# Performance work log

Hardware: AMD Instinct MI355X
Metric: run time of the kernel (lower is better)

## Reference

```python
import jax, jax.numpy as jnp
import numpy as np

B, V, C = 8192, 512, 16  # batch, num_variables, constraints per variable
N1 = V + 1  # augmented with bias column


def setup_inputs() -> dict:
    key = jax.random.key(0)
    k1, k2, k3 = jax.random.split(key, 3)
    preds = jax.random.normal(k1, (B, V), dtype=jnp.float32)
    # Acyclic structure: variable v's constraints only reference earlier
    # variables (columns < v) plus the bias column (column V).
    cols = jnp.arange(N1)[None, :]              # [1, N1]
    vids = jnp.arange(V)[:, None]               # [V, 1]
    mask = ((cols < vids) | (cols == V)).astype(jnp.float32)[:, None, :]  # [V,1,N1]
    scale = 0.1
    pos_mats = jax.random.normal(k2, (V, C, N1), dtype=jnp.float32) * scale * mask
    neg_mats = jax.random.normal(k3, (V, C, N1), dtype=jnp.float32) * scale * mask
    return {"preds": preds, "pos_mats": pos_mats, "neg_mats": neg_mats}


def reference(preds, pos_mats, neg_mats):
    # Augment preds with a ones column (bias), as in the original __call__.
    b = preds.shape[0]
    p0 = jnp.concatenate([preds, jnp.ones((b, 1), preds.dtype)], axis=1)  # [B, N1]
    var_ids = jnp.arange(pos_mats.shape[0])

    def step(p, xs):
        pm, nm, v = xs  # pm, nm: [C, N1]
        # apply_matrix: (preds * matrix).sum(-1) with max / min reduction over C
        lower = jnp.einsum('bn,cn->bc', p, pm).max(axis=1)  # [B]
        upper = jnp.einsum('bn,cn->bc', p, nm).min(axis=1)  # [B]
        # get_final_x_correction: clamp prediction into [lower, upper]
        corrected = jnp.minimum(jnp.maximum(p[:, v], lower), upper)
        p = p.at[:, v].set(corrected)
        return p, None

    pf, _ = jax.lax.scan(step, p0, (pos_mats, neg_mats, var_ids))
    return pf[:, : preds.shape[1]]
```

## Files before the change

### kernel.cpp

```cpp
#include <hip/hip_runtime.h>

#define BATCH 8192
#define V 512
#define N1 513
#define KCH 16
#define NCHUNKS 32
#define RB 32
#define NT 1024
#define PKS 520
#define SJ 516

typedef __bf16 bf16_t;
typedef bf16_t bf16x8 __attribute__((ext_vector_type(8)));
typedef float f32x4 __attribute__((ext_vector_type(4)));
typedef float f32x2 __attribute__((ext_vector_type(2)));

#define EPP 4194304ull
#define DV_OFF (EPP * 2ull)
#define BV_OFF (DV_OFF + 1048576ull)

__device__ __forceinline__ f32x4 mfma16(bf16x8 a, bf16x8 b, f32x4 c) {
    return __builtin_amdgcn_mfma_f32_16x16x32_bf16(a, b, c, 0, 0, 0);
}

__global__ __launch_bounds__(256)
void repack_all(const float* __restrict__ pos, const float* __restrict__ neg,
                bf16_t* __restrict__ Mhi, float* __restrict__ Dv,
                float* __restrict__ Bv)
{
    const int bx = blockIdx.x;
    if (bx < 496) {
        const int cc  = (bx >> 4) + 1;
        const int kb  = bx & 15;
        const int nkb = (cc + 1) >> 1;
        if (kb >= nkb) return;
        const int klen = 16 * cc;
        const size_t base = 16384ull * (size_t)((cc * cc) / 4) + (size_t)kb * 16384ull;
        for (int e = threadIdx.x; e < 16384; e += 256) {
            const int t = e >> 9, s = (e >> 3) & 63, jj = e & 7;
            const int c = s & 15, q = s >> 4;
            const int v = cc * 16 + (t >> 1);
            const int k = kb * 32 + 8 * q + jj;
            const float* src = (t & 1) ? neg : pos;
            float x = (k < klen) ? src[(size_t)(v * 16 + c) * N1 + k] : 0.0f;
            if (t & 1) x = -x;
            Mhi[base + e] = (bf16_t)x;
        }
    } else {
        const int e = (bx - 496) * 256 + threadIdx.x;
        if (e < 262144) {
            const int cc = e >> 13, vl = (e >> 9) & 15, j = e & 511;
            const int v = cc * 16 + (j >> 5), c = j & 15;
            const float* src = (j & 16) ? neg : pos;
            const float x = src[(size_t)(v * 16 + c) * N1 + cc * 16 + vl];
            Dv[e] = (j & 16) ? -x : x;
        } else {
            const int e2 = e - 262144;
            const int cc = e2 >> 9, j = e2 & 511;
            const int v = cc * 16 + (j >> 5), c = j & 15;
            const float* src = (j & 16) ? neg : pos;
            const float x = src[(size_t)(v * 16 + c) * N1 + V];
            Bv[e2] = (j & 16) ? -x : x;
        }
    }
}

__global__ __launch_bounds__(NT)
void shield_fused(const float* __restrict__ preds,
                  const bf16_t* __restrict__ Mhi,
                  const float* __restrict__ Dv, const float* __restrict__ Bv,
                  float* __restrict__ out)
{
    __shared__ bf16_t Phi[RB * PKS];
    __shared__ float  S[RB * SJ];

    const int tid  = threadIdx.x;
    const int b0   = blockIdx.x * RB;
    const int lane = tid & 63;
    const int w    = tid >> 6;
    const int cq   = lane & 15;
    const int q    = lane >> 4;
    const int rp0  = w * 2;

    {
        const int r = tid >> 5, seg = tid & 31;
        const float* prow = preds + (size_t)(b0 + r) * V + seg * 16;
        #pragma unroll
        for (int k = 0; k < 16; k += 4) {
            const float4 p4 = *(const float4*)(prow + k);
            const int n = seg * 16 + k;
            Phi[r * PKS + n + 0] = (bf16_t)p4.x;
            Phi[r * PKS + n + 1] = (bf16_t)p4.y;
            Phi[r * PKS + n + 2] = (bf16_t)p4.z;
            Phi[r * PKS + n + 3] = (bf16_t)p4.w;
        }
    }

    int tJ[2];
    #pragma unroll
    for (int tt = 0; tt < 2; ++tt) tJ[tt] = ((2 * w + tt) << 4) + cq;
    const int aoff0 = cq * PKS + 8 * q;
    const int aoff1 = (16 + cq) * PKS + 8 * q;

    f32x4 acc[2][2];
    #pragma unroll
    for (int tt = 0; tt < 2; ++tt) {
        const float b = Bv[tJ[tt]];
        acc[0][tt] = f32x4{b, b, b, b};
        acc[1][tt] = f32x4{b, b, b, b};
    }

    #pragma unroll 1
    for (int cc = 0; cc < NCHUNKS; ++cc) {
        const int v0 = cc * 16;
        const int  ccn  = cc + 1;
        const bool hasN = ccn < NCHUNKS;
        const int  nkbN = hasN ? ((ccn + 1) >> 1) : 0;
        const bf16_t* phN = Mhi + 16384ull * (size_t)((ccn * ccn) / 4)
                          + (size_t)lane * 8 + (size_t)(2 * w) * 512;

        #pragma unroll
        for (int tt = 0; tt < 2; ++tt)
            #pragma unroll
            for (int reg = 0; reg < 4; ++reg) {
                S[(4 * q + reg) * SJ + tJ[tt]]      = acc[0][tt][reg];
                S[(16 + 4 * q + reg) * SJ + tJ[tt]] = acc[1][tt][reg];
            }
        __syncthreads();

        f32x2 s2[8];
        {
            const float4 a0 = *(const float4*)(&S[rp0 * SJ + 8 * lane]);
            const float4 a1 = *(const float4*)(&S[rp0 * SJ + 8 * lane + 4]);
            const float4 c0 = *(const float4*)(&S[(rp0 + 1) * SJ + 8 * lane]);
            const float4 c1 = *(const float4*)(&S[(rp0 + 1) * SJ + 8 * lane + 4]);
            s2[0] = f32x2{a0.x, c0.x}; s2[1] = f32x2{a0.y, c0.y};
            s2[2] = f32x2{a0.z, c0.z}; s2[3] = f32x2{a0.w, c0.w};
            s2[4] = f32x2{a1.x, c1.x}; s2[5] = f32x2{a1.y, c1.y};
            s2[6] = f32x2{a1.z, c1.z}; s2[7] = f32x2{a1.w, c1.w};
        }

        if (hasN) {
            #pragma unroll
            for (int tt = 0; tt < 2; ++tt) {
                const float b = Bv[(ccn << 9) + tJ[tt]];
                acc[0][tt] = f32x4{b, b, b, b};
                acc[1][tt] = f32x4{b, b, b, b};
            }
        }

        #pragma unroll
        for (int vl = 0; vl < KCH; ++vl) {
            const int vcur = v0 + vl;
            const bool doKb = hasN && (vl < nkbN - 1);

            bf16x8 fa0, fa1, fb0, fb1;
            if (doKb) {
                const int k0 = vl * 32;
                fa0 = *(const bf16x8*)(Phi + aoff0 + k0);
                fa1 = *(const bf16x8*)(Phi + aoff1 + k0);
                const bf16_t* pb = phN + (size_t)k0 * 512;
                fb0 = *(const bf16x8*)(pb);
                fb1 = *(const bf16x8*)(pb + 512);
            }

            float dv[8], po[2];
            {
                const float* dp = Dv + ((size_t)vcur << 9) + 8 * lane;
                const float4 d0 = *(const float4*)(dp);
                const float4 d1 = *(const float4*)(dp + 4);
                dv[0]=d0.x; dv[1]=d0.y; dv[2]=d0.z; dv[3]=d0.w;
                dv[4]=d1.x; dv[5]=d1.y; dv[6]=d1.z; dv[7]=d1.w;
                po[0] = (float)Phi[rp0 * PKS + vcur];
                po[1] = (float)Phi[(rp0 + 1) * PKS + vcur];
            }

            f32x2 m01 = __builtin_elementwise_max(s2[0], s2[1]);
            f32x2 m23 = __builtin_elementwise_max(s2[2], s2[3]);
            f32x2 m45 = __builtin_elementwise_max(s2[4], s2[5]);
            f32x2 m67 = __builtin_elementwise_max(s2[6], s2[7]);
            f32x2 mx  = __builtin_elementwise_max(
                            __builtin_elementwise_max(m01, m23),
                            __builtin_elementwise_max(m45, m67));
            float red[2];
            #pragma unroll
            for (int r = 0; r < 2; ++r)
                red[r] = fmaxf(mx[r], __shfl_xor(mx[r], 1, 64));
            float pc[2];
            #pragma unroll
            for (int r = 0; r < 2; ++r) {
                const float lw  = __shfl(red[r], 4 * vl, 64);
                const float nup = __shfl(red[r], 4 * vl + 2, 64);
                pc[r] = fminf(fmaxf(po[r], lw), -nup);
            }
            if (lane == 4 * vl) {
                Phi[rp0 * PKS + vcur]       = (bf16_t)pc[0];
                Phi[(rp0 + 1) * PKS + vcur] = (bf16_t)pc[1];
            }
            const f32x2 pcv = {pc[0], pc[1]};
            #pragma unroll
            for (int jj = 0; jj < 8; ++jj) {
                const f32x2 dsp = {dv[jj], dv[jj]};
                s2[jj] = __builtin_elementwise_fma(dsp, pcv, s2[jj]);
            }

            if (doKb) {
                acc[0][0] = mfma16(fa0, fb0, acc[0][0]);
                acc[1][0] = mfma16(fa1, fb0, acc[1][0]);
                acc[0][1] = mfma16(fa0, fb1, acc[0][1]);
                acc[1][1] = mfma16(fa1, fb1, acc[1][1]);
            }
        }

        __syncthreads();

        if (hasN) {
            const int k0 = (nkbN - 1) * 32;
            const bf16x8 fa0 = *(const bf16x8*)(Phi + aoff0 + k0);
            const bf16x8 fa1 = *(const bf16x8*)(Phi + aoff1 + k0);
            const bf16_t* pb = phN + (size_t)k0 * 512;
            const bf16x8 fb0 = *(const bf16x8*)(pb);
            const bf16x8 fb1 = *(const bf16x8*)(pb + 512);
            acc[0][0] = mfma16(fa0, fb0, acc[0][0]);
            acc[1][0] = mfma16(fa1, fb0, acc[1][0]);
            acc[0][1] = mfma16(fa0, fb1, acc[0][1]);
            acc[1][1] = mfma16(fa1, fb1, acc[1][1]);
        }
    }

    {
        const int r = tid >> 5, seg = tid & 31;
        float* orow = out + (size_t)(b0 + r) * V + seg * 16;
        #pragma unroll
        for (int k = 0; k < 16; k += 4) {
            const int n = seg * 16 + k;
            float4 o;
            o.x = (float)Phi[r * PKS + n + 0];
            o.y = (float)Phi[r * PKS + n + 1];
            o.z = (float)Phi[r * PKS + n + 2];
            o.w = (float)Phi[r * PKS + n + 3];
            *(float4*)(orow + k) = o;
        }
    }
}

extern "C" void kernel_launch(void* const* d_in, const int* in_sizes, int n_in,
                              void* d_out, int out_size, void* d_ws, size_t ws_size,
                              hipStream_t stream) {
    const float* preds = (const float*)d_in[0];
    const float* pos   = (const float*)d_in[1];
    const float* neg   = (const float*)d_in[2];
    float* o = (float*)d_out;
    char* base = (char*)d_ws;
    bf16_t* Mhi = (bf16_t*)base;
    float*  Dv  = (float*)(base + DV_OFF);
    float*  Bv  = (float*)(base + BV_OFF);
    repack_all<<<dim3(1584), 256, 0, stream>>>(pos, neg, Mhi, Dv, Bv);
    shield_fused<<<dim3(BATCH / RB), NT, 0, stream>>>(preds, Mhi, Dv, Bv, o);
}
```

Measured before the change: 419.3 us.

## Use DPP/readlane reductions, padded S layout, hoisted Phi reads, LDS-staged repack

The serial per-variable critical path now uses a DPP quad-permute for the xor-1 max and readlane broadcasts instead of ds_bpermute shuffles. The original element is read once per chunk from Phi in vectors rather than from LDS at every step. The S staging buffer gets a padded stride (12 per 8 columns) to cut LDS bank conflicts on the transpose. The Dv/Bv repack is restructured to one block per chunk, staged through shared memory so global reads are coalesced, which cuts the grid from 1584 to 528 blocks. Launch bounds add a minimum-occupancy hint, and the larger S buffer raises LDS use per block.

```diff
diff --git a/kernel.cpp b/kernel.cpp
--- a/kernel.cpp
+++ b/kernel.cpp
@@ -8,7 +8,7 @@
 #define RB 32
 #define NT 1024
 #define PKS 520
-#define SJ 516
+#define SJP 772
 
 typedef __bf16 bf16_t;
 typedef bf16_t bf16x8 __attribute__((ext_vector_type(8)));
@@ -21,6 +21,17 @@
 
 __device__ __forceinline__ f32x4 mfma16(bf16x8 a, bf16x8 b, f32x4 c) {
     return __builtin_amdgcn_mfma_f32_16x16x32_bf16(a, b, c, 0, 0, 0);
+}
+
+__device__ __forceinline__ float bcast_lane(float x, int l) {
+    return __int_as_float(__builtin_amdgcn_readlane(__float_as_int(x), l));
+}
+
+__device__ __forceinline__ float dpp_xor1_max(float x) {
+    const int xi = __float_as_int(x);
+    const float o = __int_as_float(
+        __builtin_amdgcn_update_dpp(xi, xi, 0xB1, 0xF, 0xF, false));
+    return fmaxf(x, o);
 }
 
 __global__ __launch_bounds__(256)
@@ -28,6 +39,8 @@
                 bf16_t* __restrict__ Mhi, float* __restrict__ Dv,
                 float* __restrict__ Bv)
 {
+    __shared__ float bufP[256 * 17];
+    __shared__ float bufN[256 * 17];
     const int bx = blockIdx.x;
     if (bx < 496) {
         const int cc  = (bx >> 4) + 1;
@@ -47,32 +60,39 @@
             Mhi[base + e] = (bf16_t)x;
         }
     } else {
-        const int e = (bx - 496) * 256 + threadIdx.x;
-        if (e < 262144) {
-            const int cc = e >> 13, vl = (e >> 9) & 15, j = e & 511;
-            const int v = cc * 16 + (j >> 5), c = j & 15;
-            const float* src = (j & 16) ? neg : pos;
-            const float x = src[(size_t)(v * 16 + c) * N1 + cc * 16 + vl];
-            Dv[e] = (j & 16) ? -x : x;
-        } else {
-            const int e2 = e - 262144;
-            const int cc = e2 >> 9, j = e2 & 511;
-            const int v = cc * 16 + (j >> 5), c = j & 15;
-            const float* src = (j & 16) ? neg : pos;
-            const float x = src[(size_t)(v * 16 + c) * N1 + V];
-            Bv[e2] = (j & 16) ? -x : x;
-        }
-    }
-}
-
-__global__ __launch_bounds__(NT)
+        const int cc = bx - 496;
+        for (int idx = threadIdx.x; idx < 4096; idx += 256) {
+            const int r = idx >> 4, kk = idx & 15;
+            const size_t row = (size_t)(cc * 256 + r);
+            bufP[r * 17 + kk] = pos[row * N1 + cc * 16 + kk];
+            bufN[r * 17 + kk] = neg[row * N1 + cc * 16 + kk];
+        }
+        __syncthreads();
+        for (int idx = threadIdx.x; idx < 8192; idx += 256) {
+            const int vl = idx >> 9, j = idx & 511;
+            const int vlo = j >> 5, c = j & 15;
+            const int m = (j >> 4) & 1;
+            const float x = (m ? bufN : bufP)[(vlo * 16 + c) * 17 + vl];
+            Dv[(size_t)cc * 8192 + idx] = m ? -x : x;
+        }
+        for (int j = threadIdx.x; j < 512; j += 256) {
+            const int vlo = j >> 5, c = j & 15;
+            const int m = (j >> 4) & 1;
+            const float* src = m ? neg : pos;
+            const float x = src[(size_t)(cc * 256 + vlo * 16 + c) * N1 + V];
+            Bv[(size_t)cc * 512 + j] = m ? -x : x;
+        }
+    }
+}
+
+__global__ __launch_bounds__(NT, 4)
 void shield_fused(const float* __restrict__ preds,
                   const bf16_t* __restrict__ Mhi,
                   const float* __restrict__ Dv, const float* __restrict__ Bv,
                   float* __restrict__ out)
 {
     __shared__ bf16_t Phi[RB * PKS];
-    __shared__ float  S[RB * SJ];
+    __shared__ float  S[RB * SJP];
 
     const int tid  = threadIdx.x;
     const int b0   = blockIdx.x * RB;
@@ -96,9 +116,12 @@
         }
     }
 
-    int tJ[2];
+    int tJ[2], sct[2];
     #pragma unroll
-    for (int tt = 0; tt < 2; ++tt) tJ[tt] = ((2 * w + tt) << 4) + cq;
+    for (int tt = 0; tt < 2; ++tt) {
+        tJ[tt]  = ((2 * w + tt) << 4) + cq;
+        sct[tt] = 12 * (tJ[tt] >> 3) + (tJ[tt] & 7);
+    }
     const int aoff0 = cq * PKS + 8 * q;
     const int aoff1 = (16 + cq) * PKS + 8 * q;
 
@@ -123,22 +146,28 @@
         for (int tt = 0; tt < 2; ++tt)
             #pragma unroll
             for (int reg = 0; reg < 4; ++reg) {
-                S[(4 * q + reg) * SJ + tJ[tt]]      = acc[0][tt][reg];
-                S[(16 + 4 * q + reg) * SJ + tJ[tt]] = acc[1][tt][reg];
+                S[(4 * q + reg) * SJP + sct[tt]]      = acc[0][tt][reg];
+                S[(16 + 4 * q + reg) * SJP + sct[tt]] = acc[1][tt][reg];
             }
         __syncthreads();
 
         f32x2 s2[8];
         {
-            const float4 a0 = *(const float4*)(&S[rp0 * SJ + 8 * lane]);
-            const float4 a1 = *(const float4*)(&S[rp0 * SJ + 8 * lane + 4]);
-            const float4 c0 = *(const float4*)(&S[(rp0 + 1) * SJ + 8 * lane]);
-            const float4 c1 = *(const float4*)(&S[(rp0 + 1) * SJ + 8 * lane + 4]);
+            const float* sp = &S[rp0 * SJP + 12 * lane];
+            const float4 a0 = *(const float4*)(sp);
+            const float4 a1 = *(const float4*)(sp + 4);
+            const float4 c0 = *(const float4*)(sp + SJP);
+            const float4 c1 = *(const float4*)(sp + SJP + 4);
             s2[0] = f32x2{a0.x, c0.x}; s2[1] = f32x2{a0.y, c0.y};
             s2[2] = f32x2{a0.z, c0.z}; s2[3] = f32x2{a0.w, c0.w};
             s2[4] = f32x2{a1.x, c1.x}; s2[5] = f32x2{a1.y, c1.y};
             s2[6] = f32x2{a1.z, c1.z}; s2[7] = f32x2{a1.w, c1.w};
         }
+
+        const bf16x8 poA0 = *(const bf16x8*)(Phi + rp0 * PKS + v0);
+        const bf16x8 poA1 = *(const bf16x8*)(Phi + rp0 * PKS + v0 + 8);
+        const bf16x8 poB0 = *(const bf16x8*)(Phi + (rp0 + 1) * PKS + v0);
+        const bf16x8 poB1 = *(const bf16x8*)(Phi + (rp0 + 1) * PKS + v0 + 8);
 
         if (hasN) {
             #pragma unroll
@@ -164,34 +193,34 @@
                 fb1 = *(const bf16x8*)(pb + 512);
             }
 
-            float dv[8], po[2];
+            float dv[8];
             {
                 const float* dp = Dv + ((size_t)vcur << 9) + 8 * lane;
                 const float4 d0 = *(const float4*)(dp);
                 const float4 d1 = *(const float4*)(dp + 4);
                 dv[0]=d0.x; dv[1]=d0.y; dv[2]=d0.z; dv[3]=d0.w;
                 dv[4]=d1.x; dv[5]=d1.y; dv[6]=d1.z; dv[7]=d1.w;
-                po[0] = (float)Phi[rp0 * PKS + vcur];
-                po[1] = (float)Phi[(rp0 + 1) * PKS + vcur];
-            }
-
-            f32x2 m01 = __builtin_elementwise_max(s2[0], s2[1]);
-            f32x2 m23 = __builtin_elementwise_max(s2[2], s2[3]);
-            f32x2 m45 = __builtin_elementwise_max(s2[4], s2[5]);
-            f32x2 m67 = __builtin_elementwise_max(s2[6], s2[7]);
-            f32x2 mx  = __builtin_elementwise_max(
-                            __builtin_elementwise_max(m01, m23),
-                            __builtin_elementwise_max(m45, m67));
+            }
+            const float po_[2] = {
+                (float)(vl < 8 ? poA0[vl & 7] : poA1[vl & 7]),
+                (float)(vl < 8 ? poB0[vl & 7] : poB1[vl & 7])
+            };
+
             float red[2];
             #pragma unroll
-            for (int r = 0; r < 2; ++r)
-                red[r] = fmaxf(mx[r], __shfl_xor(mx[r], 1, 64));
+            for (int r = 0; r < 2; ++r) {
+                const float m0 = fmaxf(fmaxf(s2[0][r], s2[1][r]), s2[2][r]);
+                const float m1 = fmaxf(fmaxf(s2[3][r], s2[4][r]), s2[5][r]);
+                const float m2 = fmaxf(s2[6][r], s2[7][r]);
+                const float mxr = fmaxf(fmaxf(m0, m1), m2);
+                red[r] = dpp_xor1_max(mxr);
+            }
             float pc[2];
             #pragma unroll
             for (int r = 0; r < 2; ++r) {
-                const float lw  = __shfl(red[r], 4 * vl, 64);
-                const float nup = __shfl(red[r], 4 * vl + 2, 64);
-                pc[r] = fminf(fmaxf(po[r], lw), -nup);
+                const float lw  = bcast_lane(red[r], 4 * vl);
+                const float nup = bcast_lane(red[r], 4 * vl + 2);
+                pc[r] = fminf(fmaxf(po_[r], lw), -nup);
             }
             if (lane == 4 * vl) {
                 Phi[rp0 * PKS + vcur]       = (bf16_t)pc[0];
@@ -255,6 +284,6 @@
     bf16_t* Mhi = (bf16_t*)base;
     float*  Dv  = (float*)(base + DV_OFF);
     float*  Bv  = (float*)(base + BV_OFF);
-    repack_all<<<dim3(1584), 256, 0, stream>>>(pos, neg, Mhi, Dv, Bv);
+    repack_all<<<dim3(528), 256, 0, stream>>>(pos, neg, Mhi, Dv, Bv);
     shield_fused<<<dim3(BATCH / RB), NT, 0, stream>>>(preds, Mhi, Dv, Bv, o);
 }
```

Result: faster. 394.2 us (-6.0%).
